# Optimization experiments

Hardware: AMD Instinct MI355X
Metric: run time of the kernel (lower is better)

The kernel has to match this reference:

```python
import jax, jax.numpy as jnp
import numpy as np

B, Q, T, H, W = 8, 100, 50, 256, 256
COST_MASK_W = 1.0  # init kwarg cost_mask
COST_DICE_W = 1.0  # init kwarg cost_dice


def setup_inputs() -> dict:
    key = jax.random.key(0)
    k1, k2 = jax.random.split(key)
    pred_masks = jax.random.normal(k1, (B, Q, H, W), dtype=jnp.float32)
    # binary GT masks (0/1), already at prediction resolution so nearest-interp is identity
    tgt_masks = jax.random.randint(k2, (B, T, H, W), 0, 2).astype(jnp.int32)
    return {"pred_masks": pred_masks, "tgt_masks": tgt_masks}


def reference(pred_masks, tgt_masks):
    # pred_masks: [B, Q, H, W] logits; tgt_masks: [B, T, H, W] binary
    b, q = pred_masks.shape[:2]
    x = pred_masks.reshape(b, q, -1)                      # [B, Q, HW]
    t = tgt_masks.reshape(b, tgt_masks.shape[1], -1).astype(x.dtype)  # [B, T, HW]
    hw = x.shape[-1]

    # batch_sigmoid_ce_loss: BCE-with-logits vs all-ones / all-zeros targets
    pos = jax.nn.softplus(-x)                             # BCE(x, 1)
    neg = jax.nn.softplus(x)                              # BCE(x, 0)
    cost_ce = (jnp.einsum('bqc,btc->bqt', pos, t)
               + jnp.einsum('bqc,btc->bqt', neg, 1.0 - t)) / hw

    # batch_dice_loss
    s = jax.nn.sigmoid(x)
    numerator = 2.0 * jnp.einsum('bqc,btc->bqt', s, t)
    denominator = s.sum(-1)[:, :, None] + t.sum(-1)[:, None, :]
    cost_dice = 1.0 - (numerator + 1.0) / (denominator + 1.0)

    # per-batch cost matrix C [B, Q, T]; the scipy Hungarian step is a
    # host-side CPU call outside the accelerator workload.
    return COST_MASK_W * cost_ce + COST_DICE_W * cost_dice
```

## Files before the change

### kernel.cpp

```cpp
#include <hip/hip_runtime.h>
#include <math.h>

#define B_ 8
#define Q_ 100
#define T_ 50
#define HW_ 65536
#define NSEG 64
#define SEG (HW_ / NSEG)
#define KC 64
#define NCH (SEG / KC)
#define MP 101
#define NP 64
#define LDP 72

#define DSZ (B_ * MP * NP)
#define WS_D1 0
#define WS_D2 DSZ
#define WS_SNEG (2 * DSZ)
#define WS_TOTAL (2 * DSZ + B_ * Q_)

typedef __attribute__((ext_vector_type(8))) short bf16x8;
typedef __attribute__((ext_vector_type(4))) float f32x4;

__device__ __forceinline__ unsigned short f2bf(float f) {
    union { float f; unsigned u; } v; v.f = f;
    unsigned r = v.u + 0x7FFF + ((v.u >> 16) & 1);
    return (unsigned short)(r >> 16);
}

__global__ void zero_ws(float* ws) {
    int i = blockIdx.x * blockDim.x + threadIdx.x;
    if (i < WS_TOTAL) ws[i] = 0.f;
}

__global__ __launch_bounds__(256) void gemm_fused(const float* __restrict__ pred,
                                                  const int* __restrict__ tgt,
                                                  float* __restrict__ ws) {
    const int seg = blockIdx.x;
    const int b   = blockIdx.y;
    const int tid = threadIdx.x;

    __shared__ short xs[112][LDP];
    __shared__ short ss[112][LDP];
    __shared__ short ts[64][LDP];
    __shared__ float sneg_l[Q_];

    f32x4 accx[7], accs[7];
#pragma unroll
    for (int i = 0; i < 7; i++) { accx[i] = (f32x4)(0.f); accs[i] = (f32x4)(0.f); }
    float snegr[7] = {0.f, 0.f, 0.f, 0.f, 0.f, 0.f, 0.f};

    for (int i = tid; i < 12 * LDP; i += 256) {
        int r = 100 + i / LDP, c = i % LDP;
        xs[r][c] = 0;
        ss[r][c] = (r == 100) ? (short)0x3F80 : (short)0;
    }
    for (int i = tid; i < 14 * LDP; i += 256) {
        int r = 50 + i / LDP, c = i % LDP;
        ts[r][c] = (r == 50) ? (short)0x3F80 : (short)0;
    }
    if (tid < Q_) sneg_l[tid] = 0.f;

    const int lane = tid & 63;
    const int wave = tid >> 6;
    const int quad = lane >> 4;
    const int l16  = lane & 15;

    const size_t xrow0 = (size_t)b * Q_ * HW_ + (size_t)seg * SEG;
    const size_t trow0 = (size_t)b * T_ * HW_ + (size_t)seg * SEG;

    for (int ch = 0; ch < NCH; ++ch) {
        const int k0 = ch * KC;
        __syncthreads();

        {
            int j = 0;
            for (int i = tid; i < Q_ * (KC / 4); i += 256, j++) {
                int r = i >> 4, c4 = i & 15;
                float4 v = *(const float4*)(pred + xrow0 + (size_t)r * HW_ + k0 + c4 * 4);
                ushort4 xb, sb;
                float sp = 0.f;
#pragma unroll
                for (int e = 0; e < 4; e++) {
                    float x = (&v.x)[e];
                    float ax = fabsf(x);
                    float ee = __expf(-ax);
                    float d = 1.f + ee;
                    float r1 = __builtin_amdgcn_rcpf(d);
                    float sg = (x >= 0.f) ? r1 : ee * r1;
                    sp += fmaxf(x, 0.f) + 0.69314718056f * __log2f(d);
                    (&xb.x)[e] = f2bf(x);
                    (&sb.x)[e] = f2bf(sg);
                }
                snegr[j] += sp;
                *(ushort4*)&xs[r][c4 * 4] = xb;
                *(ushort4*)&ss[r][c4 * 4] = sb;
            }
        }
        for (int i = tid; i < T_ * (KC / 4); i += 256) {
            int r = i >> 4, c4 = i & 15;
            int4 v = *(const int4*)(tgt + trow0 + (size_t)r * HW_ + k0 + c4 * 4);
            ushort4 tb;
            tb.x = v.x ? 0x3F80 : 0;
            tb.y = v.y ? 0x3F80 : 0;
            tb.z = v.z ? 0x3F80 : 0;
            tb.w = v.w ? 0x3F80 : 0;
            *(ushort4*)&ts[r][c4 * 4] = tb;
        }
        __syncthreads();

#pragma unroll
        for (int kk = 0; kk < KC / 32; kk++) {
            const int kb = kk * 32 + quad * 8;
            bf16x8 bfrag = *(bf16x8*)&ts[wave * 16 + l16][kb];
#pragma unroll
            for (int mt = 0; mt < 7; mt++) {
                bf16x8 ax = *(bf16x8*)&xs[mt * 16 + l16][kb];
                bf16x8 as = *(bf16x8*)&ss[mt * 16 + l16][kb];
                accx[mt] = __builtin_amdgcn_mfma_f32_16x16x32_bf16(ax, bfrag, accx[mt], 0, 0, 0);
                accs[mt] = __builtin_amdgcn_mfma_f32_16x16x32_bf16(as, bfrag, accs[mt], 0, 0, 0);
            }
        }
    }

    {
        int j = 0;
        for (int i = tid; i < Q_ * (KC / 4); i += 256, j++) {
            int r = i >> 4;
            atomicAdd(&sneg_l[r], snegr[j]);
        }
    }
    __syncthreads();
    if (tid < Q_) atomicAdd(&ws[WS_SNEG + b * Q_ + tid], sneg_l[tid]);

    const int n = wave * 16 + l16;
#pragma unroll
    for (int mt = 0; mt < 7; mt++) {
#pragma unroll
        for (int r = 0; r < 4; r++) {
            int m = mt * 16 + quad * 4 + r;
            if (m < Q_ && n < T_)
                atomicAdd(&ws[WS_D1 + ((size_t)b * MP + m) * NP + n], accx[mt][r]);
            if (m <= Q_ && n <= T_)
                atomicAdd(&ws[WS_D2 + ((size_t)b * MP + m) * NP + n], accs[mt][r]);
        }
    }
}

__global__ void finalize(const float* __restrict__ ws, float* __restrict__ out) {
    int i = blockIdx.x * blockDim.x + threadIdx.x;
    if (i >= B_ * Q_ * T_) return;
    int b = i / (Q_ * T_);
    int r = i % (Q_ * T_);
    int q = r / T_;
    int t = r % T_;
    float dx   = ws[WS_D1 + ((size_t)b * MP + q) * NP + t];
    float ds   = ws[WS_D2 + ((size_t)b * MP + q) * NP + t];
    float ssum = ws[WS_D2 + ((size_t)b * MP + q) * NP + T_];
    float st   = ws[WS_D2 + ((size_t)b * MP + Q_) * NP + t];
    float sneg = ws[WS_SNEG + b * Q_ + q];
    float ce = (sneg - dx) * (1.f / (float)HW_);
    float dice = 1.f - (2.f * ds + 1.f) / (ssum + st + 1.f);
    out[i] = ce + dice;
}

extern "C" void kernel_launch(void* const* d_in, const int* in_sizes, int n_in,
                              void* d_out, int out_size, void* d_ws, size_t ws_size,
                              hipStream_t stream) {
    const float* pred = (const float*)d_in[0];
    const int* tgt = (const int*)d_in[1];
    float* ws = (float*)d_ws;
    float* out = (float*)d_out;

    zero_ws<<<(WS_TOTAL + 255) / 256, 256, 0, stream>>>(ws);
    dim3 g(NSEG, B_, 1);
    gemm_fused<<<g, 256, 0, stream>>>(pred, tgt, ws);
    finalize<<<(B_ * Q_ * T_ + 255) / 256, 256, 0, stream>>>(ws, out);
}
```

Measured before the change: 420.8 us.

## Load MFMA fragments directly from global memory with register double-buffering, dropping LDS staging

Each lane now loads its bf16 fragment elements straight from global memory into registers. A 2-deep register prefetch overlaps the next 32-wide k-chunk load with the current compute, which removes the shared-memory staging and the per-chunk __syncthreads barriers. The target column sums move to a separate workspace array computed from the raw targets, and a launch-bounds occupancy hint is added. In exchange, every wave reloads all target tiles (4x redundant target reads), and padded query rows 100-127 are clamped and recomputed, which wastes some transcendental work.

```diff
diff --git a/kernel.cpp b/kernel.cpp
--- a/kernel.cpp
+++ b/kernel.cpp
@@ -7,17 +7,15 @@
 #define HW_ 65536
 #define NSEG 64
 #define SEG (HW_ / NSEG)
-#define KC 64
-#define NCH (SEG / KC)
-#define MP 101
-#define NP 64
-#define LDP 72
-
-#define DSZ (B_ * MP * NP)
+#define NK32 (SEG / 32)
+#define NSTR 52
+
+#define DSZ (B_ * Q_ * NSTR)
 #define WS_D1 0
 #define WS_D2 DSZ
 #define WS_SNEG (2 * DSZ)
-#define WS_TOTAL (2 * DSZ + B_ * Q_)
+#define WS_ST (2 * DSZ + B_ * Q_)
+#define WS_TOTAL (2 * DSZ + B_ * Q_ + B_ * T_)
 
 typedef __attribute__((ext_vector_type(8))) short bf16x8;
 typedef __attribute__((ext_vector_type(4))) float f32x4;
@@ -33,116 +31,145 @@
     if (i < WS_TOTAL) ws[i] = 0.f;
 }
 
-__global__ __launch_bounds__(256) void gemm_fused(const float* __restrict__ pred,
-                                                  const int* __restrict__ tgt,
-                                                  float* __restrict__ ws) {
+__global__ __launch_bounds__(256, 2) void gemm_fused(const float* __restrict__ pred,
+                                                     const int* __restrict__ tgt,
+                                                     float* __restrict__ ws) {
     const int seg = blockIdx.x;
     const int b   = blockIdx.y;
     const int tid = threadIdx.x;
-
-    __shared__ short xs[112][LDP];
-    __shared__ short ss[112][LDP];
-    __shared__ short ts[64][LDP];
-    __shared__ float sneg_l[Q_];
-
-    f32x4 accx[7], accs[7];
-#pragma unroll
-    for (int i = 0; i < 7; i++) { accx[i] = (f32x4)(0.f); accs[i] = (f32x4)(0.f); }
-    float snegr[7] = {0.f, 0.f, 0.f, 0.f, 0.f, 0.f, 0.f};
-
-    for (int i = tid; i < 12 * LDP; i += 256) {
-        int r = 100 + i / LDP, c = i % LDP;
-        xs[r][c] = 0;
-        ss[r][c] = (r == 100) ? (short)0x3F80 : (short)0;
-    }
-    for (int i = tid; i < 14 * LDP; i += 256) {
-        int r = 50 + i / LDP, c = i % LDP;
-        ts[r][c] = (r == 50) ? (short)0x3F80 : (short)0;
-    }
-    if (tid < Q_) sneg_l[tid] = 0.f;
-
+    const int wave = tid >> 6;
     const int lane = tid & 63;
-    const int wave = tid >> 6;
     const int quad = lane >> 4;
     const int l16  = lane & 15;
 
-    const size_t xrow0 = (size_t)b * Q_ * HW_ + (size_t)seg * SEG;
-    const size_t trow0 = (size_t)b * T_ * HW_ + (size_t)seg * SEG;
-
-    for (int ch = 0; ch < NCH; ++ch) {
-        const int k0 = ch * KC;
-        __syncthreads();
-
-        {
-            int j = 0;
-            for (int i = tid; i < Q_ * (KC / 4); i += 256, j++) {
-                int r = i >> 4, c4 = i & 15;
-                float4 v = *(const float4*)(pred + xrow0 + (size_t)r * HW_ + k0 + c4 * 4);
-                ushort4 xb, sb;
-                float sp = 0.f;
-#pragma unroll
-                for (int e = 0; e < 4; e++) {
-                    float x = (&v.x)[e];
+    const float* xptr[2];
+#pragma unroll
+    for (int mt = 0; mt < 2; ++mt) {
+        int m = (wave + mt * 4) * 16 + l16;
+        int mr = m < Q_ ? m : Q_ - 1;
+        xptr[mt] = pred + ((size_t)b * Q_ + mr) * HW_ + (size_t)seg * SEG + quad * 8;
+    }
+    const int* tptr[4];
+    int ones[4];
+#pragma unroll
+    for (int nt = 0; nt < 4; ++nt) {
+        int n = nt * 16 + l16;
+        ones[nt] = (n == T_);
+        int nr = n < T_ ? n : T_ - 1;
+        tptr[nt] = tgt + ((size_t)b * T_ + nr) * HW_ + (size_t)seg * SEG + quad * 8;
+    }
+
+    f32x4 accx[2][4], accs[2][4];
+#pragma unroll
+    for (int mt = 0; mt < 2; ++mt)
+#pragma unroll
+        for (int nt = 0; nt < 4; ++nt) {
+            accx[mt][nt] = (f32x4)(0.f);
+            accs[mt][nt] = (f32x4)(0.f);
+        }
+    float sneg[2] = {0.f, 0.f};
+    float stq[4] = {0.f, 0.f, 0.f, 0.f};
+
+    float4 xrb[2][2][2];
+    int4   trb[2][4][2];
+
+    auto loadraw = [&](int ch, float4 xr[2][2], int4 tr[4][2]) {
+        const int k = ch * 32;
+#pragma unroll
+        for (int mt = 0; mt < 2; ++mt) {
+            xr[mt][0] = *(const float4*)(xptr[mt] + k);
+            xr[mt][1] = *(const float4*)(xptr[mt] + k + 4);
+        }
+#pragma unroll
+        for (int nt = 0; nt < 4; ++nt) {
+            tr[nt][0] = *(const int4*)(tptr[nt] + k);
+            tr[nt][1] = *(const int4*)(tptr[nt] + k + 4);
+        }
+    };
+
+    auto compute = [&](float4 xr[2][2], int4 tr[4][2]) {
+        bf16x8 tf[4];
+#pragma unroll
+        for (int nt = 0; nt < 4; ++nt) {
+            float cnt = 0.f;
+#pragma unroll
+            for (int h = 0; h < 2; ++h)
+#pragma unroll
+                for (int e = 0; e < 4; ++e) {
+                    int v = (&tr[nt][h].x)[e];
+                    tf[nt][h * 4 + e] = (v || ones[nt]) ? (short)0x3F80 : (short)0;
+                    cnt += v ? 1.f : 0.f;
+                }
+            stq[nt] += cnt;
+        }
+#pragma unroll
+        for (int mt = 0; mt < 2; ++mt) {
+            bf16x8 xf, sf;
+            float sp = 0.f;
+#pragma unroll
+            for (int h = 0; h < 2; ++h)
+#pragma unroll
+                for (int e = 0; e < 4; ++e) {
+                    float x = (&xr[mt][h].x)[e];
                     float ax = fabsf(x);
                     float ee = __expf(-ax);
                     float d = 1.f + ee;
                     float r1 = __builtin_amdgcn_rcpf(d);
                     float sg = (x >= 0.f) ? r1 : ee * r1;
                     sp += fmaxf(x, 0.f) + 0.69314718056f * __log2f(d);
-                    (&xb.x)[e] = f2bf(x);
-                    (&sb.x)[e] = f2bf(sg);
+                    xf[h * 4 + e] = (short)f2bf(x);
+                    sf[h * 4 + e] = (short)f2bf(sg);
                 }
-                snegr[j] += sp;
-                *(ushort4*)&xs[r][c4 * 4] = xb;
-                *(ushort4*)&ss[r][c4 * 4] = sb;
+            sneg[mt] += sp;
+#pragma unroll
+            for (int nt = 0; nt < 4; ++nt) {
+                accx[mt][nt] = __builtin_amdgcn_mfma_f32_16x16x32_bf16(xf, tf[nt], accx[mt][nt], 0, 0, 0);
+                accs[mt][nt] = __builtin_amdgcn_mfma_f32_16x16x32_bf16(sf, tf[nt], accs[mt][nt], 0, 0, 0);
             }
         }
-        for (int i = tid; i < T_ * (KC / 4); i += 256) {
-            int r = i >> 4, c4 = i & 15;
-            int4 v = *(const int4*)(tgt + trow0 + (size_t)r * HW_ + k0 + c4 * 4);
-            ushort4 tb;
-            tb.x = v.x ? 0x3F80 : 0;
-            tb.y = v.y ? 0x3F80 : 0;
-            tb.z = v.z ? 0x3F80 : 0;
-            tb.w = v.w ? 0x3F80 : 0;
-            *(ushort4*)&ts[r][c4 * 4] = tb;
-        }
-        __syncthreads();
-
-#pragma unroll
-        for (int kk = 0; kk < KC / 32; kk++) {
-            const int kb = kk * 32 + quad * 8;
-            bf16x8 bfrag = *(bf16x8*)&ts[wave * 16 + l16][kb];
-#pragma unroll
-            for (int mt = 0; mt < 7; mt++) {
-                bf16x8 ax = *(bf16x8*)&xs[mt * 16 + l16][kb];
-                bf16x8 as = *(bf16x8*)&ss[mt * 16 + l16][kb];
-                accx[mt] = __builtin_amdgcn_mfma_f32_16x16x32_bf16(ax, bfrag, accx[mt], 0, 0, 0);
-                accs[mt] = __builtin_amdgcn_mfma_f32_16x16x32_bf16(as, bfrag, accs[mt], 0, 0, 0);
+    };
+
+    loadraw(0, xrb[0], trb[0]);
+#pragma unroll 2
+    for (int ch = 0; ch < NK32; ++ch) {
+        const int cb = ch & 1;
+        if (ch + 1 < NK32) loadraw(ch + 1, xrb[cb ^ 1], trb[cb ^ 1]);
+        compute(xrb[cb], trb[cb]);
+    }
+
+#pragma unroll
+    for (int mt = 0; mt < 2; ++mt) {
+        float v = sneg[mt];
+        v += __shfl_xor(v, 16);
+        v += __shfl_xor(v, 32);
+        int m = (wave + mt * 4) * 16 + l16;
+        if (quad == 0 && m < Q_) atomicAdd(&ws[WS_SNEG + b * Q_ + m], v);
+    }
+    if (wave == 0) {
+#pragma unroll
+        for (int nt = 0; nt < 4; ++nt) {
+            float v = stq[nt];
+            v += __shfl_xor(v, 16);
+            v += __shfl_xor(v, 32);
+            int n = nt * 16 + l16;
+            if (quad == 0 && n < T_) atomicAdd(&ws[WS_ST + b * T_ + n], v);
+        }
+    }
+#pragma unroll
+    for (int mt = 0; mt < 2; ++mt) {
+        int mtile = (wave + mt * 4) * 16;
+#pragma unroll
+        for (int nt = 0; nt < 4; ++nt) {
+            int n = nt * 16 + l16;
+#pragma unroll
+            for (int r = 0; r < 4; ++r) {
+                int m = mtile + quad * 4 + r;
+                if (m < Q_) {
+                    size_t idx = ((size_t)b * Q_ + m) * NSTR + n;
+                    if (n < T_) atomicAdd(&ws[WS_D1 + idx], accx[mt][nt][r]);
+                    if (n <= T_) atomicAdd(&ws[WS_D2 + idx], accs[mt][nt][r]);
+                }
             }
-        }
-    }
-
-    {
-        int j = 0;
-        for (int i = tid; i < Q_ * (KC / 4); i += 256, j++) {
-            int r = i >> 4;
-            atomicAdd(&sneg_l[r], snegr[j]);
-        }
-    }
-    __syncthreads();
-    if (tid < Q_) atomicAdd(&ws[WS_SNEG + b * Q_ + tid], sneg_l[tid]);
-
-    const int n = wave * 16 + l16;
-#pragma unroll
-    for (int mt = 0; mt < 7; mt++) {
-#pragma unroll
-        for (int r = 0; r < 4; r++) {
-            int m = mt * 16 + quad * 4 + r;
-            if (m < Q_ && n < T_)
-                atomicAdd(&ws[WS_D1 + ((size_t)b * MP + m) * NP + n], accx[mt][r]);
-            if (m <= Q_ && n <= T_)
-                atomicAdd(&ws[WS_D2 + ((size_t)b * MP + m) * NP + n], accs[mt][r]);
         }
     }
 }
@@ -154,10 +181,10 @@
     int r = i % (Q_ * T_);
     int q = r / T_;
     int t = r % T_;
-    float dx   = ws[WS_D1 + ((size_t)b * MP + q) * NP + t];
-    float ds   = ws[WS_D2 + ((size_t)b * MP + q) * NP + t];
-    float ssum = ws[WS_D2 + ((size_t)b * MP + q) * NP + T_];
-    float st   = ws[WS_D2 + ((size_t)b * MP + Q_) * NP + t];
+    float dx   = ws[WS_D1 + ((size_t)b * Q_ + q) * NSTR + t];
+    float ds   = ws[WS_D2 + ((size_t)b * Q_ + q) * NSTR + t];
+    float ssum = ws[WS_D2 + ((size_t)b * Q_ + q) * NSTR + T_];
+    float st   = ws[WS_ST + b * T_ + t];
     float sneg = ws[WS_SNEG + b * Q_ + q];
     float ce = (sneg - dx) * (1.f / (float)HW_);
     float dice = 1.f - (2.f * ds + 1.f) / (ssum + st + 1.f);
```

New measurement: 398.1 us. 5.4% less time.
